# Performance work log

Measured on AMD Instinct MI355X. Metric: run time of the kernel, lower is better.

The kernel has to match this reference:

```python
import jax, jax.numpy as jnp
import numpy as np

USR_NUM = 100000
D_IN = 32
D_HID = 32
D_MID = 16
D_OUT = 2
N_EDGES = 1600000
EPS = 1e-16  # matches torch_geometric.utils.softmax denominator eps


def _glorot(key, shape):
    fan_in, fan_out = shape[0], shape[1]
    lim = np.sqrt(6.0 / (fan_in + fan_out))
    return jax.random.uniform(key, shape, jnp.float32, -lim, lim)


def setup_inputs() -> dict:
    key = jax.random.key(0)
    ks = jax.random.split(key, 16)
    inp = {
        "edge_index": jax.random.randint(ks[0], (2, N_EDGES), 0, USR_NUM, dtype=jnp.int64)
        if jax.config.jax_enable_x64 else jax.random.randint(ks[0], (2, N_EDGES), 0, USR_NUM).astype(jnp.int32),
        "emb": jax.random.normal(ks[1], (USR_NUM, D_IN), jnp.float32),
        # conv1: TransformerConv(32 -> 32, heads=1)
        "Wq1": _glorot(ks[2], (D_IN, D_HID)), "bq1": jnp.zeros((D_HID,), jnp.float32),
        "Wk1": _glorot(ks[3], (D_IN, D_HID)), "bk1": jnp.zeros((D_HID,), jnp.float32),
        "Wv1": _glorot(ks[4], (D_IN, D_HID)), "bv1": jnp.zeros((D_HID,), jnp.float32),
        "Ws1": _glorot(ks[5], (D_IN, D_HID)), "bs1": jnp.zeros((D_HID,), jnp.float32),
        # conv2: TransformerConv(32 -> 16, heads=1)
        "Wq2": _glorot(ks[6], (D_HID, D_MID)), "bq2": jnp.zeros((D_MID,), jnp.float32),
        "Wk2": _glorot(ks[7], (D_HID, D_MID)), "bk2": jnp.zeros((D_MID,), jnp.float32),
        "Wv2": _glorot(ks[8], (D_HID, D_MID)), "bv2": jnp.zeros((D_MID,), jnp.float32),
        "Ws2": _glorot(ks[9], (D_HID, D_MID)), "bs2": jnp.zeros((D_MID,), jnp.float32),
        # output: Linear(16 -> 2)
        "Wo": _glorot(ks[10], (D_MID, D_OUT)), "bo": jnp.zeros((D_OUT,), jnp.float32),
    }
    return inp


def transformer_conv(x, src, dst, Wq, bq, Wk, bk, Wv, bv, Ws, bs, n_nodes):
    # edge (j=src -> i=dst): alpha_ij = softmax_i( <q_i, k_j> / sqrt(d) )
    d = Wq.shape[1]
    q = (x @ Wq + bq)[dst]          # [E, d]
    k = (x @ Wk + bk)[src]          # [E, d]
    v = (x @ Wv + bv)[src]          # [E, d]
    alpha = jnp.sum(q * k, axis=-1) / jnp.sqrt(jnp.float32(d))  # [E]
    # segment softmax over incoming edges of each destination node
    seg_max = jax.ops.segment_max(alpha, dst, num_segments=n_nodes)  # [N]
    e = jnp.exp(alpha - seg_max[dst])
    seg_sum = jax.ops.segment_sum(e, dst, num_segments=n_nodes)      # [N]
    w = e / (seg_sum[dst] + EPS)
    agg = jax.ops.segment_sum(v * w[:, None], dst, num_segments=n_nodes)  # [N, d]
    return agg + x @ Ws + bs  # root/skip connection (PyG default root_weight=True)


def reference(edge_index, emb,
              Wq1, bq1, Wk1, bk1, Wv1, bv1, Ws1, bs1,
              Wq2, bq2, Wk2, bk2, Wv2, bv2, Ws2, bs2,
              Wo, bo):
    src, dst = edge_index[0], edge_index[1]
    h = transformer_conv(emb, src, dst, Wq1, bq1, Wk1, bk1, Wv1, bv1, Ws1, bs1, USR_NUM)
    h = jax.nn.relu(h)
    h = transformer_conv(h, src, dst, Wq2, bq2, Wk2, bk2, Wv2, bv2, Ws2, bs2, USR_NUM)
    h = jax.nn.relu(h)
    return h @ Wo + bo  # [N, 2]
```

## Files before the change

kernel.cpp:

```cpp
#include <hip/hip_runtime.h>
#include <hip/hip_bf16.h>

typedef __hip_bfloat16 bf16;
typedef unsigned int uint;
typedef unsigned short ushort;

#define N_NODES 100000
#define N_EDGES_C 1600000
#define NSB2 1568
#define NSB2P 1792
#define SCAN_E 7
#define RND 2048
#define EPB (RND / 256)
#define NBIN 64
#define G_RAD ((N_EDGES_C + RND - 1) / RND)
#define HCAP 1536
#define NSLOT (NSB2 * 64)
#define NCHUNK 8
#define KEYN (64 * NCHUNK)

__device__ __forceinline__ float ldf(const void* p, long i, int isbf) {
    return isbf ? __bfloat162float(((const bf16*)p)[i]) : ((const float*)p)[i];
}
__device__ __forceinline__ int ldidx(const int* ei, long pos, int is64) {
    return is64 ? ei[2 * pos] : ei[pos];
}
__device__ __forceinline__ ushort bfb(float x) {
    bf16 h = __float2bfloat16(x);
    return *(ushort*)&h;
}
__device__ __forceinline__ float bl(uint u) { return __uint_as_float(u << 16); }
__device__ __forceinline__ float bh(uint u) { return __uint_as_float(u & 0xFFFF0000u); }

__global__ void setup_kernel(
    const void* emb, const int* ei,
    const void* Wq1, const void* bq1, const void* Wk1, const void* bk1,
    const void* Wv1, const void* bv1, const void* Ws1, const void* bs1,
    const void* Wq2, const void* bq2, const void* Wk2, const void* bk2,
    const void* Wv2, const void* bv2, const void* Ws2, const void* bs2,
    const void* Wo, const void* bo,
    int* flags, float* wp1, float* bp1, float* wp2, float* bp2, float* woF,
    int* curSB) {
    __shared__ int sf0;
    int t = threadIdx.x;
    if (t < 64) {
        const bf16* pb = (const bf16*)emb;
        int bad = 0;
        for (int i = t; i < 256; i += 64) {
            float v = __bfloat162float(pb[i]);
            if (!(v > -1.0e6f && v < 1.0e6f)) bad++;
        }
        int nz = 0;
        for (int i = 2 * t + 1; i < 256; i += 128) nz += (ei[i] != 0) ? 1 : 0;
#pragma unroll
        for (int m = 32; m >= 1; m >>= 1) {
            bad += __shfl_xor(bad, m, 64);
            nz  += __shfl_xor(nz, m, 64);
        }
        if (t == 0) {
            int f0 = (bad <= 8) ? 1 : 0;
            flags[0] = f0;
            flags[1] = (nz == 0) ? 1 : 0;
            sf0 = f0;
        }
    }
    __syncthreads();
    int isbf = sf0;
    for (int i = t; i < 1024; i += 256) {
        wp1[i]        = ldf(Wq1, i, isbf);
        wp1[1024 + i] = ldf(Wk1, i, isbf);
        wp1[2048 + i] = ldf(Wv1, i, isbf);
        wp1[3072 + i] = ldf(Ws1, i, isbf);
    }
    for (int i = t; i < 512; i += 256) {
        wp2[i]        = ldf(Wq2, i, isbf);
        wp2[512 + i]  = ldf(Wk2, i, isbf);
        wp2[1024 + i] = ldf(Wv2, i, isbf);
        wp2[1536 + i] = ldf(Ws2, i, isbf);
    }
    if (t < 32) {
        bp1[t] = ldf(bq1, t, isbf); bp1[32 + t] = ldf(bk1, t, isbf);
        bp1[64 + t] = ldf(bv1, t, isbf); bp1[96 + t] = ldf(bs1, t, isbf);
        woF[t] = ldf(Wo, t, isbf);
    }
    if (t < 16) {
        bp2[t] = ldf(bq2, t, isbf); bp2[16 + t] = ldf(bk2, t, isbf);
        bp2[32 + t] = ldf(bv2, t, isbf); bp2[48 + t] = ldf(bs2, t, isbf);
    }
    if (t < 2) woF[32 + t] = ldf(bo, t, isbf);
    for (int i = t; i < NSB2P; i += 256) curSB[i] = 0;
}

template <int DOUT, bool RUNTIME_DTYPE>
__device__ __forceinline__ void node_linear_body(
    const void* __restrict__ X, const float* __restrict__ wpack,
    const float* __restrict__ bpack, const int* __restrict__ flags,
    float* __restrict__ q, ushort* __restrict__ kvb, float* __restrict__ s,
    int bid, float* __restrict__ sW, float* __restrict__ sbias, float* __restrict__ sX) {
    const int TPN = DOUT / 4;
    const int NPB = 256 / TPN;
    const int W_ELEMS = 4 * 32 * DOUT;

    const float4* wp4 = (const float4*)wpack;
    float4* sW4 = (float4*)sW;
    for (int i = threadIdx.x; i < W_ELEMS / 4; i += 256) sW4[i] = wp4[i];
    if (threadIdx.x < 4 * DOUT) sbias[threadIdx.x] = bpack[threadIdx.x];
    const int base = bid * NPB * 32;
    bool useBf = RUNTIME_DTYPE && (flags[0] != 0);
    if (useBf) {
        for (int i = threadIdx.x; i < NPB * 32; i += 256) {
            int g = base + i;
            float xv = (g < N_NODES * 32) ? __bfloat162float(((const bf16*)X)[g]) : 0.0f;
            sX[(i >> 5) * 36 + (i & 31)] = xv;
        }
    } else {
        for (int i = threadIdx.x; i < NPB * 32; i += 256) {
            int g = base + i;
            sX[(i >> 5) * 36 + (i & 31)] = (g < N_NODES * 32) ? ((const float*)X)[g] : 0.0f;
        }
    }
    __syncthreads();

    int l = threadIdx.x / TPN;
    int c4 = (threadIdx.x % TPN) * 4;
    int n = bid * NPB + l;
    if (n >= N_NODES) return;

    float xr[32];
#pragma unroll
    for (int j = 0; j < 8; j++) {
        float4 t4 = *(const float4*)&sX[l * 36 + 4 * j];
        xr[4 * j] = t4.x; xr[4 * j + 1] = t4.y; xr[4 * j + 2] = t4.z; xr[4 * j + 3] = t4.w;
    }
    float acc[4][4];
#pragma unroll
    for (int m = 0; m < 4; m++)
#pragma unroll
        for (int j = 0; j < 4; j++) acc[m][j] = sbias[m * DOUT + c4 + j];

#pragma unroll
    for (int t = 0; t < 32; t++) {
#pragma unroll
        for (int m = 0; m < 4; m++) {
            float4 w = *(const float4*)&sW[(m * 32 + t) * DOUT + c4];
            acc[m][0] += xr[t] * w.x;
            acc[m][1] += xr[t] * w.y;
            acc[m][2] += xr[t] * w.z;
            acc[m][3] += xr[t] * w.w;
        }
    }
    size_t o = (size_t)n * DOUT + c4;
    *(float4*)&q[o] = make_float4(acc[0][0], acc[0][1], acc[0][2], acc[0][3]);
    *(float4*)&s[o] = make_float4(acc[3][0], acc[3][1], acc[3][2], acc[3][3]);
    size_t okv = (size_t)n * 2 * DOUT + c4;
    ushort4 kp = make_ushort4(bfb(acc[1][0]), bfb(acc[1][1]), bfb(acc[1][2]), bfb(acc[1][3]));
    ushort4 vp = make_ushort4(bfb(acc[2][0]), bfb(acc[2][1]), bfb(acc[2][2]), bfb(acc[2][3]));
    *(ushort4*)&kvb[okv]        = kp;
    *(ushort4*)&kvb[okv + DOUT] = vp;
}

struct RadixS {
    int cnt[NSB2P]; int excl[NSB2P]; int gbase[NSB2P]; int wsum[4];
    uint sVal[RND]; ushort sSb[RND];
};
struct LinS { float sW[4096]; float sbias[128]; float sX[32 * 36]; };
union alignas(16) FusedS { RadixS r; LinS l; };

__global__ void __launch_bounds__(256, 4) fused_ra_nl(
    const int* __restrict__ ei, const int* __restrict__ flags,
    int* __restrict__ curSB, uint* __restrict__ pairsSB,
    const void* __restrict__ X, const float* __restrict__ wpack,
    const float* __restrict__ bpack,
    float* __restrict__ q, ushort* __restrict__ kvb, float* __restrict__ s) {
    __shared__ FusedS u;
    if (blockIdx.x >= G_RAD) {
        node_linear_body<32, true>(X, wpack, bpack, flags, q, kvb, s,
                                   (int)blockIdx.x - G_RAD, u.l.sW, u.l.sbias, u.l.sX);
        return;
    }
    int* cnt = u.r.cnt; int* excl = u.r.excl; int* gbase = u.r.gbase;
    uint* sVal = u.r.sVal; ushort* sSb = u.r.sSb;
    const int is64 = flags[1];
    int t = threadIdx.x;
    for (int i = t; i < NSB2P; i += 256) cnt[i] = 0;
    __syncthreads();
    long base = (long)blockIdx.x * RND;

    int mySb[EPB]; int myRank[EPB]; uint myPk[EPB];
#pragma unroll
    for (int r = 0; r < EPB; r++) {
        long e = base + r * 256 + t;
        mySb[r] = -1;
        if (e < N_EDGES_C) {
            int d = ldidx(ei, (long)N_EDGES_C + e, is64);
            int src = ldidx(ei, e, is64);
            int sb = d >> 6;
            myPk[r] = (uint)src | ((uint)(d & 63) << 17);
            myRank[r] = atomicAdd(&cnt[sb], 1);
            mySb[r] = sb;
        }
    }
    __syncthreads();
    const int b7 = t * SCAN_E;
    int pre[SCAN_E];
    int s7 = 0;
#pragma unroll
    for (int j = 0; j < SCAN_E; j++) { pre[j] = s7; s7 += cnt[b7 + j]; }
    int lane6 = t & 63, wid6 = t >> 6;
    int x = s7;
#pragma unroll
    for (int off = 1; off < 64; off <<= 1) {
        int u2 = __shfl_up(x, off, 64);
        if (lane6 >= off) x += u2;
    }
    if (lane6 == 63) u.r.wsum[wid6] = x;
    __syncthreads();
    int wbase = 0;
#pragma unroll
    for (int w = 0; w < 4; w++) if (w < wid6) wbase += u.r.wsum[w];
    int basex = wbase + x - s7;
#pragma unroll
    for (int j = 0; j < SCAN_E; j++) excl[b7 + j] = basex + pre[j];
    __syncthreads();
#pragma unroll
    for (int r = 0; r < EPB; r++) {
        if (mySb[r] >= 0) {
            int pos = excl[mySb[r]] + myRank[r];
            sVal[pos] = myPk[r];
            sSb[pos] = (ushort)mySb[r];
        }
    }
    for (int i = t; i < NSB2P; i += 256)
        gbase[i] = (cnt[i] > 0) ? atomicAdd(&curSB[i], cnt[i]) : 0;
    __syncthreads();
    int tot = excl[NSB2P - 1] + cnt[NSB2P - 1];
    for (int i = t; i < tot; i += 256) {
        int sb = sSb[i];
        int gp = gbase[sb] + (i - excl[sb]);
        if (gp < HCAP)
            pairsSB[(size_t)sb * HCAP + gp] = sVal[i];
    }
}

__global__ void radix_b(
    const int* __restrict__ curSB, const uint* __restrict__ pairsSB,
    int* __restrict__ esrc,
    int* __restrict__ rowbeg, int* __restrict__ rowend,
    int* __restrict__ perm) {
    __shared__ uint sP[HCAP];
    __shared__ int dcnt[KEYN];
    __shared__ int dexcl[KEYN];
    __shared__ int hbin[NBIN], hbase[NBIN], hcur[NBIN];
    int sbh = blockIdx.x;
    int t = threadIdx.x;
    int n = min(curSB[sbh], HCAP);
    for (int i = t; i < KEYN; i += 256) dcnt[i] = 0;
    if (t < NBIN) { hbin[t] = 0; hcur[t] = 0; }
    if (t < 64) perm[sbh * 64 + t] = -1;
    __syncthreads();
    const uint* srcp = pairsSB + (size_t)sbh * HCAP;
    for (int i = t; i < n; i += 256) {
        uint pk = srcp[i];
        sP[i] = pk;
        int key = (int)((pk >> 17) & 63) * NCHUNK + (int)((pk & 0x1FFFFu) >> 14);
        atomicAdd(&dcnt[key], 1);
    }
    __syncthreads();
    int v = 0, myExcl = 0, mybin = -1;
    if (t < 64) {
        const int kb = t * NCHUNK;
        int sum = 0;
#pragma unroll
        for (int j = 0; j < NCHUNK; j++) sum += dcnt[kb + j];
        v = sum;
        int x = v;
#pragma unroll
        for (int off = 1; off < 64; off <<= 1) {
            int u2 = __shfl_up(x, off, 64);
            if (t >= off) x += u2;
        }
        myExcl = x - v;
        int run = myExcl;
#pragma unroll
        for (int j = 0; j < NCHUNK; j++) { dexcl[kb + j] = run; run += dcnt[kb + j]; }
        int dst = sbh * 64 + t;
        if (dst < N_NODES) {
            const int EB = sbh * HCAP;
            rowbeg[dst] = EB + min(myExcl, HCAP);
            rowend[dst] = EB + min(myExcl + v, HCAP);
            mybin = min(v, NBIN - 1);
            atomicAdd(&hbin[mybin], 1);
        }
    }
    __syncthreads();
    if (t < 64) {
        int hv = hbin[t];
        int sfx = hv;
#pragma unroll
        for (int off = 1; off < 64; off <<= 1) {
            int u2 = __shfl_down(sfx, off, 64);
            if (t + off < 64) sfx += u2;
        }
        hbase[t] = sfx - hv;
    }
    __syncthreads();
    if (t < 64 && mybin >= 0) {
        int r = atomicAdd(&hcur[mybin], 1);
        perm[sbh * 64 + hbase[mybin] + r] = sbh * 64 + t;
    }
    const int EB = sbh * HCAP;
    for (int i = t; i < n; i += 256) {
        uint pk = sP[i];
        int key = (int)((pk >> 17) & 63) * NCHUNK + (int)((pk & 0x1FFFFu) >> 14);
        int p2 = atomicAdd(&dexcl[key], 1);
        if (p2 < HCAP) esrc[EB + p2] = (int)(pk & 0x1FFFF);
    }
}

__global__ void gather_attn_l1(const int* __restrict__ perm,
                               const int* __restrict__ rowbeg, const int* __restrict__ rowend,
                               const int* __restrict__ esrc,
                               const float* __restrict__ q, const ushort* __restrict__ kvb,
                               const float* __restrict__ s,
                               const float* __restrict__ wp2,
                               const float* __restrict__ bp2,
                               float* __restrict__ q2o, ushort* __restrict__ kvb2o,
                               float* __restrict__ s2o) {
    const int D = 32;
    const int LPD = 4;
    const int G = 16;
    __shared__ float sW2[2048];
    __shared__ float sb2[64];
    __shared__ float sH[64 * 36];
    __shared__ int sDst[64];

    for (int i = threadIdx.x; i < 2048; i += 256) sW2[i] = wp2[i];
    if (threadIdx.x < 64) sb2[threadIdx.x] = bp2[threadIdx.x];

    int lane = threadIdx.x & 63;
    int wave = (blockIdx.x * blockDim.x + threadIdx.x) >> 6;
    int g = lane / LPD;
    int c = lane % LPD;
    int idx = wave * G + g;
    int dst = perm[idx];
    bool alive = (dst >= 0);

    const float rsq = 0.17677669529663689f;
    float4 qa = make_float4(0.f, 0.f, 0.f, 0.f), qb = qa;
    int beg = 0, end = 0;
    if (alive) {
        qa = *(const float4*)(q + (size_t)dst * D + 8 * c);
        qb = *(const float4*)(q + (size_t)dst * D + 8 * c + 4);
        beg = rowbeg[dst]; end = rowend[dst];
    }

    const char* kvbase = (const char*)kvb;
    const int ROW = 4 * D;
    const int koff = 16 * c;
    const int voff = 2 * D + 16 * c;

    float sum0 = 0.f, sum1 = 0.f;
    float a0[8] = {0,0,0,0,0,0,0,0};
    float a1[8] = {0,0,0,0,0,0,0,0};

    uint4 kq[4], vq[4];
#pragma unroll
    for (int r = 0; r < 4; r++) {
        int sn = (beg + r < end) ? esrc[beg + r] : 0;
        const char* p = kvbase + (size_t)sn * ROW;
        kq[r] = *(const uint4*)(p + koff);
        vq[r] = *(const uint4*)(p + voff);
    }

    for (int e = beg; e < end; e += 4) {
        uint4 kc[4], vc[4];
#pragma unroll
        for (int r = 0; r < 4; r++) { kc[r] = kq[r]; vc[r] = vq[r]; }
#pragma unroll
        for (int r = 0; r < 4; r++) {
            if (e + 4 + r < end) {
                const char* p = kvbase + (size_t)esrc[e + 4 + r] * ROW;
                kq[r] = *(const uint4*)(p + koff);
                vq[r] = *(const uint4*)(p + voff);
            }
        }
#pragma unroll
        for (int r = 0; r < 4; r++) {
            if (e + r < end) {
                uint4 kA = kc[r], vA = vc[r];
                float pd = qa.x * bl(kA.x) + qa.y * bh(kA.x) + qa.z * bl(kA.y) + qa.w * bh(kA.y)
                         + qb.x * bl(kA.z) + qb.y * bh(kA.z) + qb.z * bl(kA.w) + qb.w * bh(kA.w);
#pragma unroll
                for (int m = LPD / 2; m >= 1; m >>= 1) pd += __shfl_xor(pd, m, LPD);
                float ex = __expf(fminf(fmaxf(pd * rsq, -80.0f), 80.0f));
                if (r & 1) {
                    sum1 += ex;
                    a1[0] += bl(vA.x) * ex; a1[1] += bh(vA.x) * ex;
                    a1[2] += bl(vA.y) * ex; a1[3] += bh(vA.y) * ex;
                    a1[4] += bl(vA.z) * ex; a1[5] += bh(vA.z) * ex;
                    a1[6] += bl(vA.w) * ex; a1[7] += bh(vA.w) * ex;
                } else {
                    sum0 += ex;
                    a0[0] += bl(vA.x) * ex; a0[1] += bh(vA.x) * ex;
                    a0[2] += bl(vA.y) * ex; a0[3] += bh(vA.y) * ex;
                    a0[4] += bl(vA.z) * ex; a0[5] += bh(vA.z) * ex;
                    a0[6] += bl(vA.w) * ex; a0[7] += bh(vA.w) * ex;
                }
            }
        }
    }
    float inv = 1.0f / (sum0 + sum1 + 1e-16f);
    float4 sa = make_float4(0.f, 0.f, 0.f, 0.f), sbv = sa;
    if (alive) {
        sa  = *(const float4*)(s + (size_t)dst * D + 8 * c);
        sbv = *(const float4*)(s + (size_t)dst * D + 8 * c + 4);
    }
    float h[8];
    h[0] = (a0[0] + a1[0]) * inv + sa.x;  h[1] = (a0[1] + a1[1]) * inv + sa.y;
    h[2] = (a0[2] + a1[2]) * inv + sa.z;  h[3] = (a0[3] + a1[3]) * inv + sa.w;
    h[4] = (a0[4] + a1[4]) * inv + sbv.x; h[5] = (a0[5] + a1[5]) * inv + sbv.y;
    h[6] = (a0[6] + a1[6]) * inv + sbv.z; h[7] = (a0[7] + a1[7]) * inv + sbv.w;
#pragma unroll
    for (int j = 0; j < 8; j++) h[j] = h[j] > 0.0f ? h[j] : 0.0f;

    int gl = (threadIdx.x >> 6) * G + g;
    if (alive) {
        *(float4*)&sH[gl * 36 + 8 * c]     = make_float4(h[0], h[1], h[2], h[3]);
        *(float4*)&sH[gl * 36 + 8 * c + 4] = make_float4(h[4], h[5], h[6], h[7]);
    }
    if (c == 0) sDst[gl] = dst;
    __syncthreads();
    int l = threadIdx.x >> 2;
    int c4 = (threadIdx.x & 3) * 4;
    int nd = sDst[l];
    if (nd >= 0) {
        float acc2[4][4];
#pragma unroll
        for (int m = 0; m < 4; m++)
#pragma unroll
            for (int j = 0; j < 4; j++) acc2[m][j] = sb2[m * 16 + c4 + j];
#pragma unroll
        for (int t2 = 0; t2 < 32; t2++) {
            float xv = sH[l * 36 + t2];
#pragma unroll
            for (int m = 0; m < 4; m++) {
                float4 w = *(const float4*)&sW2[(m * 32 + t2) * 16 + c4];
                acc2[m][0] += xv * w.x;
                acc2[m][1] += xv * w.y;
                acc2[m][2] += xv * w.z;
                acc2[m][3] += xv * w.w;
            }
        }
        size_t o = (size_t)nd * 16 + c4;
        *(float4*)&q2o[o] = make_float4(acc2[0][0], acc2[0][1], acc2[0][2], acc2[0][3]);
        *(float4*)&s2o[o] = make_float4(acc2[3][0], acc2[3][1], acc2[3][2], acc2[3][3]);
        size_t okv = (size_t)nd * 32 + c4;
        ushort4 kp = make_ushort4(bfb(acc2[1][0]), bfb(acc2[1][1]), bfb(acc2[1][2]), bfb(acc2[1][3]));
        ushort4 vp = make_ushort4(bfb(acc2[2][0]), bfb(acc2[2][1]), bfb(acc2[2][2]), bfb(acc2[2][3]));
        *(ushort4*)&kvb2o[okv]      = kp;
        *(ushort4*)&kvb2o[okv + 16] = vp;
    }
}

__global__ void gather_attn_l2(const int* __restrict__ perm,
                               const int* __restrict__ rowbeg, const int* __restrict__ rowend,
                               const int* __restrict__ esrc,
                               const float* __restrict__ q, const ushort* __restrict__ kvb,
                               const float* __restrict__ s,
                               const float* __restrict__ woF,
                               const int* __restrict__ flags,
                               void* __restrict__ out) {
    const int D = 16;
    const int LG = 4;
    const int KL = 2;
    const int G  = 16;

    int lane = threadIdx.x & 63;
    int W = (blockIdx.x * blockDim.x + threadIdx.x) >> 6;
    int g = lane / LG;
    int sub = lane % LG;
    bool isK = (sub < KL);
    int cv = sub - KL;
    int idx = W * G + g;
    int dst = perm[idx];
    if (dst < 0) return;

    const float rsq = 0.25f;
    float qacc[8] = {0,0,0,0,0,0,0,0};
    if (isK) {
        float4 qa = *(const float4*)(q + (size_t)dst * D + 8 * sub);
        float4 qb = *(const float4*)(q + (size_t)dst * D + 8 * sub + 4);
        qacc[0] = qa.x; qacc[1] = qa.y; qacc[2] = qa.z; qacc[3] = qa.w;
        qacc[4] = qb.x; qacc[5] = qb.y; qacc[6] = qb.z; qacc[7] = qb.w;
    }
    int beg = rowbeg[dst], end = rowend[dst];

    const char* kvbase = (const char*)kvb + 16 * sub;
    const int ROW = 4 * D;

    float sum = 0.f;

    uint4 rv[4];
    int sn1[4];
#pragma unroll
    for (int r = 0; r < 4; r++) {
        int sn = (beg + r < end) ? esrc[beg + r] : 0;
        rv[r] = *(const uint4*)(kvbase + (size_t)sn * ROW);
    }
#pragma unroll
    for (int r = 0; r < 4; r++)
        sn1[r] = (beg + 4 + r < end) ? esrc[beg + 4 + r] : 0;

    for (int e = beg; e < end; e += 4) {
        uint4 rc[4];
#pragma unroll
        for (int r = 0; r < 4; r++) rc[r] = rv[r];
#pragma unroll
        for (int r = 0; r < 4; r++) {
            if (e + 4 + r < end)
                rv[r] = *(const uint4*)(kvbase + (size_t)sn1[r] * ROW);
        }
#pragma unroll
        for (int r = 0; r < 4; r++) {
            if (e + 8 + r < end) sn1[r] = esrc[e + 8 + r];
        }
#pragma unroll
        for (int r = 0; r < 4; r++) {
            if (e + r < end) {
                uint4 rA = rc[r];
                float pd = 0.f;
                if (isK) {
                    pd = qacc[0] * bl(rA.x) + qacc[1] * bh(rA.x)
                       + qacc[2] * bl(rA.y) + qacc[3] * bh(rA.y)
                       + qacc[4] * bl(rA.z) + qacc[5] * bh(rA.z)
                       + qacc[6] * bl(rA.w) + qacc[7] * bh(rA.w);
                }
                pd += __shfl_xor(pd, 1, KL);
                float pdx = __shfl_xor(pd, KL, LG);
                float pdf = isK ? pd : pdx;
                float ex = __expf(fminf(fmaxf(pdf * rsq, -80.0f), 80.0f));
                sum += ex;
                if (!isK) {
                    qacc[0] += bl(rA.x) * ex; qacc[1] += bh(rA.x) * ex;
                    qacc[2] += bl(rA.y) * ex; qacc[3] += bh(rA.y) * ex;
                    qacc[4] += bl(rA.z) * ex; qacc[5] += bh(rA.z) * ex;
                    qacc[6] += bl(rA.w) * ex; qacc[7] += bh(rA.w) * ex;
                }
            }
        }
    }
    float inv = 1.0f / (sum + 1e-16f);
    float p0 = 0.f, p1 = 0.f;
    if (!isK) {
        float4 sa  = *(const float4*)(s + (size_t)dst * D + 8 * cv);
        float4 sbv = *(const float4*)(s + (size_t)dst * D + 8 * cv + 4);
        float h[8];
        h[0] = qacc[0] * inv + sa.x;  h[1] = qacc[1] * inv + sa.y;
        h[2] = qacc[2] * inv + sa.z;  h[3] = qacc[3] * inv + sa.w;
        h[4] = qacc[4] * inv + sbv.x; h[5] = qacc[5] * inv + sbv.y;
        h[6] = qacc[6] * inv + sbv.z; h[7] = qacc[7] * inv + sbv.w;
#pragma unroll
        for (int j = 0; j < 8; j++) h[j] = h[j] > 0.0f ? h[j] : 0.0f;
#pragma unroll
        for (int j = 0; j < 8; j++) {
            p0 += h[j] * woF[(8 * cv + j) * 2 + 0];
            p1 += h[j] * woF[(8 * cv + j) * 2 + 1];
        }
    }
    p0 += __shfl_xor(p0, 1, 2);
    p1 += __shfl_xor(p1, 1, 2);
    if (sub == KL) {
        float o0 = p0 + woF[32];
        float o1 = p1 + woF[33];
        if (flags[0]) {
            ((bf16*)out)[dst * 2 + 0] = __float2bfloat16(o0);
            ((bf16*)out)[dst * 2 + 1] = __float2bfloat16(o1);
        } else {
            ((float*)out)[dst * 2 + 0] = o0;
            ((float*)out)[dst * 2 + 1] = o1;
        }
    }
}

extern "C" void kernel_launch(void* const* d_in, const int* in_sizes, int n_in,
                              void* d_out, int out_size, void* d_ws, size_t ws_size,
                              hipStream_t stream) {
    const int* ei  = (const int*)d_in[0];
    const void* emb = d_in[1];
    const void *Wq1 = d_in[2],  *bq1 = d_in[3];
    const void *Wk1 = d_in[4],  *bk1 = d_in[5];
    const void *Wv1 = d_in[6],  *bv1 = d_in[7];
    const void *Ws1 = d_in[8],  *bs1 = d_in[9];
    const void *Wq2 = d_in[10], *bq2 = d_in[11];
    const void *Wk2 = d_in[12], *bk2 = d_in[13];
    const void *Wv2 = d_in[14], *bv2 = d_in[15];
    const void *Ws2 = d_in[16], *bs2 = d_in[17];
    const void *Wo  = d_in[18], *bo  = d_in[19];

    const size_t ND   = (size_t)N_NODES * 32;
    const size_t ND16 = (size_t)N_NODES * 16;
    const size_t SBTOT = (size_t)NSB2 * HCAP;
    float* base   = (float*)d_ws;
    int*   flags  = (int*)base;
    float* wp1    = base + 64;
    float* bp1    = wp1 + 4096;
    float* wp2    = bp1 + 128;
    float* bp2    = wp2 + 2048;
    float* woF    = bp2 + 64;
    int*   curSB  = (int*)(woF + 64);
    int*   rowbeg = curSB + NSB2P;
    int*   rowend = rowbeg + N_NODES;
    int*   perm   = rowend + N_NODES;
    float* p      = (float*)(perm + NSLOT);
    p = (float*)(((uintptr_t)p + 127) & ~(uintptr_t)127);
    float* q      = p; p += ND;
    float* s      = p; p += ND;
    ushort* kvb   = (ushort*)p; p += ND;
    float* q2     = p; p += ND16;
    float* s2     = p; p += ND16;
    ushort* kvb2  = (ushort*)p; p += ND16;
    int*   esrc   = (int*)p; p += SBTOT;
    uint*  pairsSB = (uint*)p;

    const int B = 256;
    const int gNL32  = (N_NODES + 31) / 32;
    const int gFused = G_RAD + gNL32;
    const int gG1    = NSLOT / 64;
    const int gG2    = NSLOT / 64;

    setup_kernel<<<1, B, 0, stream>>>(emb, ei,
        Wq1, bq1, Wk1, bk1, Wv1, bv1, Ws1, bs1,
        Wq2, bq2, Wk2, bk2, Wv2, bv2, Ws2, bs2, Wo, bo,
        flags, wp1, bp1, wp2, bp2, woF, curSB);

    fused_ra_nl<<<gFused, B, 0, stream>>>(ei, flags, curSB, pairsSB,
                                          emb, wp1, bp1, q, kvb, s);

    radix_b<<<NSB2, B, 0, stream>>>(curSB, pairsSB, esrc, rowbeg, rowend, perm);

    gather_attn_l1<<<gG1, B, 0, stream>>>(
        perm, rowbeg, rowend, esrc, q, kvb, s, wp2, bp2, q2, kvb2, s2);

    gather_attn_l2<<<gG2, B, 0, stream>>>(
        perm, rowbeg, rowend, esrc, q2, kvb2, s2, woF, flags, d_out);
}
```

Baseline: 258.5 us.

## Fuse per-superbucket CSR build into both attention gather kernels

Removes the separate radix_b kernel and rebuilds each 64-destination bucket's CSR (counts, row offsets, degree-sorted perm, source list) in shared memory at the start of each gather kernel. The first scatter pass also drops its local shared-memory sort and writes packed pairs directly to global bucket slots. This saves one launch and the global esrc/rowbeg/rowend/perm traffic, but the bucket sort is now done twice, shared memory per block grows, and the direct scatter writes are less coalesced.

New measurement: 241.9 us. 1.07x faster.

```diff
diff --git a/kernel.cpp b/kernel.cpp
--- a/kernel.cpp
+++ b/kernel.cpp
@@ -9,7 +9,6 @@
 #define N_EDGES_C 1600000
 #define NSB2 1568
 #define NSB2P 1792
-#define SCAN_E 7
 #define RND 2048
 #define EPB (RND / 256)
 #define NBIN 64
@@ -31,6 +30,72 @@
 }
 __device__ __forceinline__ float bl(uint u) { return __uint_as_float(u << 16); }
 __device__ __forceinline__ float bh(uint u) { return __uint_as_float(u & 0xFFFF0000u); }
+
+struct BuildS { int dcnt[KEYN]; int dexcl[KEYN]; int hbin[NBIN]; int hbase[NBIN]; int hcur[NBIN]; };
+
+__device__ __forceinline__ void build_csr(
+    int sbh, int n, const uint* __restrict__ srcp,
+    BuildS* b, int* sEsrc, int* sRB, int* sRE, int* sPerm) {
+    int t = threadIdx.x;
+    for (int i = t; i < KEYN; i += 256) b->dcnt[i] = 0;
+    if (t < NBIN) { b->hbin[t] = 0; b->hcur[t] = 0; }
+    if (t < 64) sPerm[t] = -1;
+    __syncthreads();
+    for (int i = t; i < n; i += 256) {
+        uint pk = srcp[i];
+        int key = (int)((pk >> 17) & 63) * NCHUNK + (int)((pk & 0x1FFFFu) >> 14);
+        atomicAdd(&b->dcnt[key], 1);
+    }
+    __syncthreads();
+    int mybin = -1;
+    if (t < 64) {
+        const int kb = t * NCHUNK;
+        int sum = 0;
+#pragma unroll
+        for (int j = 0; j < NCHUNK; j++) sum += b->dcnt[kb + j];
+        int v = sum;
+        int x = v;
+#pragma unroll
+        for (int off = 1; off < 64; off <<= 1) {
+            int u2 = __shfl_up(x, off, 64);
+            if (t >= off) x += u2;
+        }
+        int myExcl = x - v;
+        int run = myExcl;
+#pragma unroll
+        for (int j = 0; j < NCHUNK; j++) { b->dexcl[kb + j] = run; run += b->dcnt[kb + j]; }
+        sRB[t] = myExcl;
+        sRE[t] = myExcl + v;
+        int dst = sbh * 64 + t;
+        if (dst < N_NODES) {
+            mybin = min(v, NBIN - 1);
+            atomicAdd(&b->hbin[mybin], 1);
+        }
+    }
+    __syncthreads();
+    if (t < 64) {
+        int hv = b->hbin[t];
+        int sfx = hv;
+#pragma unroll
+        for (int off = 1; off < 64; off <<= 1) {
+            int u2 = __shfl_down(sfx, off, 64);
+            if (t + off < 64) sfx += u2;
+        }
+        b->hbase[t] = sfx - hv;
+    }
+    __syncthreads();
+    if (t < 64 && mybin >= 0) {
+        int r = atomicAdd(&b->hcur[mybin], 1);
+        sPerm[b->hbase[mybin] + r] = t;
+    }
+    for (int i = t; i < n; i += 256) {
+        uint pk = srcp[i];
+        int key = (int)((pk >> 17) & 63) * NCHUNK + (int)((pk & 0x1FFFFu) >> 14);
+        int p2 = atomicAdd(&b->dexcl[key], 1);
+        sEsrc[p2] = (int)(pk & 0x1FFFF);
+    }
+    __syncthreads();
+}
 
 __global__ void setup_kernel(
     const void* emb, const int* ei,
@@ -159,10 +224,7 @@
     *(ushort4*)&kvb[okv + DOUT] = vp;
 }
 
-struct RadixS {
-    int cnt[NSB2P]; int excl[NSB2P]; int gbase[NSB2P]; int wsum[4];
-    uint sVal[RND]; ushort sSb[RND];
-};
+struct RadixS { int cnt[NSB2P]; int gbase[NSB2P]; };
 struct LinS { float sW[4096]; float sbias[128]; float sX[32 * 36]; };
 union alignas(16) FusedS { RadixS r; LinS l; };
 
@@ -178,8 +240,7 @@
                                    (int)blockIdx.x - G_RAD, u.l.sW, u.l.sbias, u.l.sX);
         return;
     }
-    int* cnt = u.r.cnt; int* excl = u.r.excl; int* gbase = u.r.gbase;
-    uint* sVal = u.r.sVal; ushort* sSb = u.r.sSb;
+    int* cnt = u.r.cnt; int* gbase = u.r.gbase;
     const int is64 = flags[1];
     int t = threadIdx.x;
     for (int i = t; i < NSB2P; i += 256) cnt[i] = 0;
@@ -201,125 +262,20 @@
         }
     }
     __syncthreads();
-    const int b7 = t * SCAN_E;
-    int pre[SCAN_E];
-    int s7 = 0;
-#pragma unroll
-    for (int j = 0; j < SCAN_E; j++) { pre[j] = s7; s7 += cnt[b7 + j]; }
-    int lane6 = t & 63, wid6 = t >> 6;
-    int x = s7;
-#pragma unroll
-    for (int off = 1; off < 64; off <<= 1) {
-        int u2 = __shfl_up(x, off, 64);
-        if (lane6 >= off) x += u2;
-    }
-    if (lane6 == 63) u.r.wsum[wid6] = x;
-    __syncthreads();
-    int wbase = 0;
-#pragma unroll
-    for (int w = 0; w < 4; w++) if (w < wid6) wbase += u.r.wsum[w];
-    int basex = wbase + x - s7;
-#pragma unroll
-    for (int j = 0; j < SCAN_E; j++) excl[b7 + j] = basex + pre[j];
+    for (int i = t; i < NSB2P; i += 256)
+        gbase[i] = (cnt[i] > 0) ? atomicAdd(&curSB[i], cnt[i]) : 0;
     __syncthreads();
 #pragma unroll
     for (int r = 0; r < EPB; r++) {
         if (mySb[r] >= 0) {
-            int pos = excl[mySb[r]] + myRank[r];
-            sVal[pos] = myPk[r];
-            sSb[pos] = (ushort)mySb[r];
-        }
-    }
-    for (int i = t; i < NSB2P; i += 256)
-        gbase[i] = (cnt[i] > 0) ? atomicAdd(&curSB[i], cnt[i]) : 0;
-    __syncthreads();
-    int tot = excl[NSB2P - 1] + cnt[NSB2P - 1];
-    for (int i = t; i < tot; i += 256) {
-        int sb = sSb[i];
-        int gp = gbase[sb] + (i - excl[sb]);
-        if (gp < HCAP)
-            pairsSB[(size_t)sb * HCAP + gp] = sVal[i];
-    }
-}
-
-__global__ void radix_b(
-    const int* __restrict__ curSB, const uint* __restrict__ pairsSB,
-    int* __restrict__ esrc,
-    int* __restrict__ rowbeg, int* __restrict__ rowend,
-    int* __restrict__ perm) {
-    __shared__ uint sP[HCAP];
-    __shared__ int dcnt[KEYN];
-    __shared__ int dexcl[KEYN];
-    __shared__ int hbin[NBIN], hbase[NBIN], hcur[NBIN];
-    int sbh = blockIdx.x;
-    int t = threadIdx.x;
-    int n = min(curSB[sbh], HCAP);
-    for (int i = t; i < KEYN; i += 256) dcnt[i] = 0;
-    if (t < NBIN) { hbin[t] = 0; hcur[t] = 0; }
-    if (t < 64) perm[sbh * 64 + t] = -1;
-    __syncthreads();
-    const uint* srcp = pairsSB + (size_t)sbh * HCAP;
-    for (int i = t; i < n; i += 256) {
-        uint pk = srcp[i];
-        sP[i] = pk;
-        int key = (int)((pk >> 17) & 63) * NCHUNK + (int)((pk & 0x1FFFFu) >> 14);
-        atomicAdd(&dcnt[key], 1);
-    }
-    __syncthreads();
-    int v = 0, myExcl = 0, mybin = -1;
-    if (t < 64) {
-        const int kb = t * NCHUNK;
-        int sum = 0;
-#pragma unroll
-        for (int j = 0; j < NCHUNK; j++) sum += dcnt[kb + j];
-        v = sum;
-        int x = v;
-#pragma unroll
-        for (int off = 1; off < 64; off <<= 1) {
-            int u2 = __shfl_up(x, off, 64);
-            if (t >= off) x += u2;
-        }
-        myExcl = x - v;
-        int run = myExcl;
-#pragma unroll
-        for (int j = 0; j < NCHUNK; j++) { dexcl[kb + j] = run; run += dcnt[kb + j]; }
-        int dst = sbh * 64 + t;
-        if (dst < N_NODES) {
-            const int EB = sbh * HCAP;
-            rowbeg[dst] = EB + min(myExcl, HCAP);
-            rowend[dst] = EB + min(myExcl + v, HCAP);
-            mybin = min(v, NBIN - 1);
-            atomicAdd(&hbin[mybin], 1);
-        }
-    }
-    __syncthreads();
-    if (t < 64) {
-        int hv = hbin[t];
-        int sfx = hv;
-#pragma unroll
-        for (int off = 1; off < 64; off <<= 1) {
-            int u2 = __shfl_down(sfx, off, 64);
-            if (t + off < 64) sfx += u2;
-        }
-        hbase[t] = sfx - hv;
-    }
-    __syncthreads();
-    if (t < 64 && mybin >= 0) {
-        int r = atomicAdd(&hcur[mybin], 1);
-        perm[sbh * 64 + hbase[mybin] + r] = sbh * 64 + t;
-    }
-    const int EB = sbh * HCAP;
-    for (int i = t; i < n; i += 256) {
-        uint pk = sP[i];
-        int key = (int)((pk >> 17) & 63) * NCHUNK + (int)((pk & 0x1FFFFu) >> 14);
-        int p2 = atomicAdd(&dexcl[key], 1);
-        if (p2 < HCAP) esrc[EB + p2] = (int)(pk & 0x1FFFF);
-    }
-}
-
-__global__ void gather_attn_l1(const int* __restrict__ perm,
-                               const int* __restrict__ rowbeg, const int* __restrict__ rowend,
-                               const int* __restrict__ esrc,
+            int gp = gbase[mySb[r]] + myRank[r];
+            if (gp < HCAP)
+                pairsSB[(size_t)mySb[r] * HCAP + gp] = myPk[r];
+        }
+    }
+}
+
+__global__ void gather_attn_l1(const int* __restrict__ curSB, const uint* __restrict__ pairsSB,
                                const float* __restrict__ q, const ushort* __restrict__ kvb,
                                const float* __restrict__ s,
                                const float* __restrict__ wp2,
@@ -331,19 +287,25 @@
     const int G = 16;
     __shared__ float sW2[2048];
     __shared__ float sb2[64];
-    __shared__ float sH[64 * 36];
-    __shared__ int sDst[64];
-
+    union GU { BuildS b; float sH[64 * 36]; };
+    __shared__ GU gu;
+    __shared__ int sEsrc[HCAP];
+    __shared__ int sDst[64], sPerm[64], sRB[64], sRE[64];
+
+    int sbh = blockIdx.x;
+    int n = min(curSB[sbh], HCAP);
     for (int i = threadIdx.x; i < 2048; i += 256) sW2[i] = wp2[i];
     if (threadIdx.x < 64) sb2[threadIdx.x] = bp2[threadIdx.x];
+    build_csr(sbh, n, pairsSB + (size_t)sbh * HCAP, &gu.b, sEsrc, sRB, sRE, sPerm);
 
     int lane = threadIdx.x & 63;
-    int wave = (blockIdx.x * blockDim.x + threadIdx.x) >> 6;
+    int wave = threadIdx.x >> 6;
     int g = lane / LPD;
     int c = lane % LPD;
-    int idx = wave * G + g;
-    int dst = perm[idx];
-    bool alive = (dst >= 0);
+    int rank = wave * G + g;
+    int dl = sPerm[rank];
+    bool alive = (dl >= 0);
+    int dst = sbh * 64 + dl;
 
     const float rsq = 0.17677669529663689f;
     float4 qa = make_float4(0.f, 0.f, 0.f, 0.f), qb = qa;
@@ -351,7 +313,7 @@
     if (alive) {
         qa = *(const float4*)(q + (size_t)dst * D + 8 * c);
         qb = *(const float4*)(q + (size_t)dst * D + 8 * c + 4);
-        beg = rowbeg[dst]; end = rowend[dst];
+        beg = sRB[dl]; end = sRE[dl];
     }
 
     const char* kvbase = (const char*)kvb;
@@ -366,7 +328,7 @@
     uint4 kq[4], vq[4];
 #pragma unroll
     for (int r = 0; r < 4; r++) {
-        int sn = (beg + r < end) ? esrc[beg + r] : 0;
+        int sn = (beg + r < end) ? sEsrc[beg + r] : 0;
         const char* p = kvbase + (size_t)sn * ROW;
         kq[r] = *(const uint4*)(p + koff);
         vq[r] = *(const uint4*)(p + voff);
@@ -379,7 +341,7 @@
 #pragma unroll
         for (int r = 0; r < 4; r++) {
             if (e + 4 + r < end) {
-                const char* p = kvbase + (size_t)esrc[e + 4 + r] * ROW;
+                const char* p = kvbase + (size_t)sEsrc[e + 4 + r] * ROW;
                 kq[r] = *(const uint4*)(p + koff);
                 vq[r] = *(const uint4*)(p + voff);
             }
@@ -423,12 +385,12 @@
 #pragma unroll
     for (int j = 0; j < 8; j++) h[j] = h[j] > 0.0f ? h[j] : 0.0f;
 
-    int gl = (threadIdx.x >> 6) * G + g;
+    int gl = wave * G + g;
     if (alive) {
-        *(float4*)&sH[gl * 36 + 8 * c]     = make_float4(h[0], h[1], h[2], h[3]);
-        *(float4*)&sH[gl * 36 + 8 * c + 4] = make_float4(h[4], h[5], h[6], h[7]);
-    }
-    if (c == 0) sDst[gl] = dst;
+        *(float4*)&gu.sH[gl * 36 + 8 * c]     = make_float4(h[0], h[1], h[2], h[3]);
+        *(float4*)&gu.sH[gl * 36 + 8 * c + 4] = make_float4(h[4], h[5], h[6], h[7]);
+    }
+    if (c == 0) sDst[gl] = alive ? dst : -1;
     __syncthreads();
     int l = threadIdx.x >> 2;
     int c4 = (threadIdx.x & 3) * 4;
@@ -441,7 +403,7 @@
             for (int j = 0; j < 4; j++) acc2[m][j] = sb2[m * 16 + c4 + j];
 #pragma unroll
         for (int t2 = 0; t2 < 32; t2++) {
-            float xv = sH[l * 36 + t2];
+            float xv = gu.sH[l * 36 + t2];
 #pragma unroll
             for (int m = 0; m < 4; m++) {
                 float4 w = *(const float4*)&sW2[(m * 32 + t2) * 16 + c4];
@@ -462,9 +424,7 @@
     }
 }
 
-__global__ void gather_attn_l2(const int* __restrict__ perm,
-                               const int* __restrict__ rowbeg, const int* __restrict__ rowend,
-                               const int* __restrict__ esrc,
+__global__ void gather_attn_l2(const int* __restrict__ curSB, const uint* __restrict__ pairsSB,
                                const float* __restrict__ q, const ushort* __restrict__ kvb,
                                const float* __restrict__ s,
                                const float* __restrict__ woF,
@@ -474,16 +434,24 @@
     const int LG = 4;
     const int KL = 2;
     const int G  = 16;
+    __shared__ BuildS bs;
+    __shared__ int sEsrc[HCAP];
+    __shared__ int sPerm[64], sRB[64], sRE[64];
+
+    int sbh = blockIdx.x;
+    int n = min(curSB[sbh], HCAP);
+    build_csr(sbh, n, pairsSB + (size_t)sbh * HCAP, &bs, sEsrc, sRB, sRE, sPerm);
 
     int lane = threadIdx.x & 63;
-    int W = (blockIdx.x * blockDim.x + threadIdx.x) >> 6;
+    int wave = threadIdx.x >> 6;
     int g = lane / LG;
     int sub = lane % LG;
     bool isK = (sub < KL);
     int cv = sub - KL;
-    int idx = W * G + g;
-    int dst = perm[idx];
-    if (dst < 0) return;
+    int rank = wave * G + g;
+    int dl = sPerm[rank];
+    if (dl < 0) return;
+    int dst = sbh * 64 + dl;
 
     const float rsq = 0.25f;
     float qacc[8] = {0,0,0,0,0,0,0,0};
@@ -493,7 +461,7 @@
         qacc[0] = qa.x; qacc[1] = qa.y; qacc[2] = qa.z; qacc[3] = qa.w;
         qacc[4] = qb.x; qacc[5] = qb.y; qacc[6] = qb.z; qacc[7] = qb.w;
     }
-    int beg = rowbeg[dst], end = rowend[dst];
+    int beg = sRB[dl], end = sRE[dl];
 
     const char* kvbase = (const char*)kvb + 16 * sub;
     const int ROW = 4 * D;
@@ -504,12 +472,12 @@
     int sn1[4];
 #pragma unroll
     for (int r = 0; r < 4; r++) {
-        int sn = (beg + r < end) ? esrc[beg + r] : 0;
+        int sn = (beg + r < end) ? sEsrc[beg + r] : 0;
         rv[r] = *(const uint4*)(kvbase + (size_t)sn * ROW);
     }
 #pragma unroll
     for (int r = 0; r < 4; r++)
-        sn1[r] = (beg + 4 + r < end) ? esrc[beg + 4 + r] : 0;
+        sn1[r] = (beg + 4 + r < end) ? sEsrc[beg + 4 + r] : 0;
 
     for (int e = beg; e < end; e += 4) {
         uint4 rc[4];
@@ -522,7 +490,7 @@
         }
 #pragma unroll
         for (int r = 0; r < 4; r++) {
-            if (e + 8 + r < end) sn1[r] = esrc[e + 8 + r];
+            if (e + 8 + r < end) sn1[r] = sEsrc[e + 8 + r];
         }
 #pragma unroll
         for (int r = 0; r < 4; r++) {
@@ -608,10 +576,7 @@
     float* bp2    = wp2 + 2048;
     float* woF    = bp2 + 64;
     int*   curSB  = (int*)(woF + 64);
-    int*   rowbeg = curSB + NSB2P;
-    int*   rowend = rowbeg + N_NODES;
-    int*   perm   = rowend + N_NODES;
-    float* p      = (float*)(perm + NSLOT);
+    float* p      = (float*)(curSB + NSB2P);
     p = (float*)(((uintptr_t)p + 127) & ~(uintptr_t)127);
     float* q      = p; p += ND;
     float* s      = p; p += ND;
@@ -619,14 +584,11 @@
     float* q2     = p; p += ND16;
     float* s2     = p; p += ND16;
     ushort* kvb2  = (ushort*)p; p += ND16;
-    int*   esrc   = (int*)p; p += SBTOT;
     uint*  pairsSB = (uint*)p;
 
     const int B = 256;
     const int gNL32  = (N_NODES + 31) / 32;
     const int gFused = G_RAD + gNL32;
-    const int gG1    = NSLOT / 64;
-    const int gG2    = NSLOT / 64;
 
     setup_kernel<<<1, B, 0, stream>>>(emb, ei,
         Wq1, bq1, Wk1, bk1, Wv1, bv1, Ws1, bs1,
@@ -636,11 +598,9 @@
     fused_ra_nl<<<gFused, B, 0, stream>>>(ei, flags, curSB, pairsSB,
                                           emb, wp1, bp1, q, kvb, s);
 
-    radix_b<<<NSB2, B, 0, stream>>>(curSB, pairsSB, esrc, rowbeg, rowend, perm);
-
-    gather_attn_l1<<<gG1, B, 0, stream>>>(
-        perm, rowbeg, rowend, esrc, q, kvb, s, wp2, bp2, q2, kvb2, s2);
-
-    gather_attn_l2<<<gG2, B, 0, stream>>>(
-        perm, rowbeg, rowend, esrc, q2, kvb2, s2, woF, flags, d_out);
-}
+    gather_attn_l1<<<NSB2, B, 0, stream>>>(
+        curSB, pairsSB, q, kvb, s, wp2, bp2, q2, kvb2, s2);
+
+    gather_attn_l2<<<NSB2, B, 0, stream>>>(
+        curSB, pairsSB, q2, kvb2, s2, woF, flags, d_out);
+}
```
